# Kernel tuning notes

Hardware: AMD Instinct MI355X
Metric: run time of the kernel (lower is better)

The kernel has to match this reference:

```python
import jax, jax.numpy as jnp
import numpy as np

KEY_DIM = 1024
VALUE_DIM = 1024
NUM_HEADS = 16
ORIGIN_SHAPE = (8, 16, 16)  # T, H, W video-token grid
LOCAL_BLOCKS = 3
B = 1
S = int(np.prod(ORIGIN_SHAPE))  # 2048
DH = KEY_DIM // NUM_HEADS       # 64
DV = VALUE_DIM // NUM_HEADS


def make_layout():
    """Vectorized equivalent of SparseAttention.make_layout (causal=True)."""
    shape = np.array(ORIGIN_SHAPE, dtype=np.int64)
    cum = np.concatenate([np.flip(np.cumprod(np.flip(shape)))[1:], [1]]).astype(np.int64)
    idx = np.arange(S, dtype=np.int64)
    coords = (idx[None, :] // cum[:, None]) % shape[:, None]  # [ndim, S]
    diff = idx[:, None] - idx[None, :]
    layout = (diff >= 0) & (diff <= LOCAL_BLOCKS)  # causal local window
    for d in range(len(ORIGIN_SHAPE) - 1):  # causal axial strides along dims 0..ndim-2
        same = np.ones((S, S), dtype=bool)
        for e in range(len(ORIGIN_SHAPE)):
            if e != d:
                same &= coords[e][:, None] == coords[e][None, :]
        layout |= same & (coords[d][None, :] <= coords[d][:, None])
    return layout  # [S, S] bool


def setup_inputs() -> dict:
    key = jax.random.key(0)
    ks = jax.random.split(key, 11)
    sc = 0.02
    inp = {
        "query": jax.random.normal(ks[0], (B, S, KEY_DIM), jnp.float32),
        "key":   jax.random.normal(ks[1], (B, S, KEY_DIM), jnp.float32),
        "value": jax.random.normal(ks[2], (B, S, VALUE_DIM), jnp.float32),
        "wq": sc * jax.random.normal(ks[3], (KEY_DIM, KEY_DIM), jnp.float32),
        "bq": jnp.zeros((KEY_DIM,), jnp.float32),
        "wk": sc * jax.random.normal(ks[4], (KEY_DIM, KEY_DIM), jnp.float32),
        "bk": jnp.zeros((KEY_DIM,), jnp.float32),
        "wv": sc * jax.random.normal(ks[5], (VALUE_DIM, VALUE_DIM), jnp.float32),
        "bv": jnp.zeros((VALUE_DIM,), jnp.float32),
        "wo": sc * jax.random.normal(ks[6], (VALUE_DIM, KEY_DIM), jnp.float32),
        "bo": jnp.zeros((KEY_DIM,), jnp.float32),
        "layout": jnp.asarray(make_layout(), jnp.int32)[None, None],  # [1,1,S,S]
    }
    return inp


def reference(query, key, value, wq, bq, wk, bk, wv, bv, wo, bo, layout):
    def split(x, d):  # [B,S,H*d] -> [B,H,S,d]
        return x.reshape(B, S, NUM_HEADS, d).transpose(0, 2, 1, 3)
    q = split(query @ wq + bq, DH)
    k = split(key @ wk + bk, DH)
    v = split(value @ wv + bv, DV)
    logits = jnp.einsum('bhsd,bhtd->bhst', q, k) / jnp.sqrt(jnp.float32(DH))
    logits = jnp.where(layout > 0, logits, jnp.float32(-1e9))
    attn = jax.nn.softmax(logits, axis=-1)  # matches tf.sparse.softmax over layout support
    out = jnp.einsum('bhst,bhtd->bhsd', attn, v)
    out = out.transpose(0, 2, 1, 3).reshape(B, S, VALUE_DIM)
    return out @ wo + bo
```

## Files before the change

kernel.cpp:

```cpp
#include <hip/hip_runtime.h>
#include <hip/hip_bf16.h>
#include <cstdint>
#include <math.h>

#define SEQ    2048
#define DMODEL 1024
#define NHEAD  16
#define DHEAD  64
#define NZPAD  32

typedef __bf16 bf16;
typedef __bf16 bf16x8 __attribute__((ext_vector_type(8)));
typedef float  f32x4  __attribute__((ext_vector_type(4)));

typedef __attribute__((address_space(3))) uint32_t lds_u32;
typedef __attribute__((address_space(1))) const uint32_t global_u32;

__device__ __forceinline__ void async_load16(const void* g, void* l) {
    __builtin_amdgcn_global_load_lds((global_u32*)g, (lds_u32*)l, 16, 0, 0);
}

#define CAST_BLOCKS 3072
#define TR_BLOCKS   4096
#define NZ_BLOCKS   256

__global__ __launch_bounds__(256) void prep_kernel(
    const float* __restrict__ q, const float* __restrict__ k, const float* __restrict__ v,
    bf16* __restrict__ qx, bf16* __restrict__ kx, bf16* __restrict__ vx,
    const float* __restrict__ w0, const float* __restrict__ w1,
    const float* __restrict__ w2, const float* __restrict__ w3,
    bf16* __restrict__ t0, bf16* __restrict__ t1,
    bf16* __restrict__ t2, bf16* __restrict__ t3,
    int* __restrict__ nzidx, int* __restrict__ nzcnt) {
    __shared__ float tile[32][33];
    const int bid = blockIdx.x;
    if (bid < CAST_BLOCKS) {
        const int z = bid >> 10;
        const float* src = (z == 0) ? q : (z == 1) ? k : v;
        bf16* dst        = (z == 0) ? qx : (z == 1) ? kx : vx;
        const int i = (bid & 1023) * 256 + threadIdx.x;
        const float4* s4 = (const float4*)src;
        float4 a = s4[i * 2 + 0];
        float4 b = s4[i * 2 + 1];
        bf16x8 o;
        o[0] = (bf16)a.x; o[1] = (bf16)a.y; o[2] = (bf16)a.z; o[3] = (bf16)a.w;
        o[4] = (bf16)b.x; o[5] = (bf16)b.y; o[6] = (bf16)b.z; o[7] = (bf16)b.w;
        ((bf16x8*)dst)[i] = o;
    } else if (bid < CAST_BLOCKS + TR_BLOCKS) {
        const int b = bid - CAST_BLOCKS;
        const int z = b >> 10, rem = b & 1023;
        const float* w = (z == 0) ? w0 : (z == 1) ? w1 : (z == 2) ? w2 : w3;
        bf16* t        = (z == 0) ? t0 : (z == 1) ? t1 : (z == 2) ? t2 : t3;
        const int tx = threadIdx.x & 31, ty = threadIdx.x >> 5;
        const int kbase = (rem >> 5) * 32, nbase = (rem & 31) * 32;
#pragma unroll
        for (int i = 0; i < 4; ++i)
            tile[ty + 8 * i][tx] = w[(size_t)(kbase + ty + 8 * i) * DMODEL + nbase + tx];
        __syncthreads();
#pragma unroll
        for (int i = 0; i < 4; ++i)
            t[(size_t)(nbase + ty + 8 * i) * DMODEL + kbase + tx] = (bf16)tile[tx][ty + 8 * i];
    } else {
        const int b = bid - CAST_BLOCKS - TR_BLOCKS;
        const int g = threadIdx.x >> 5, l = threadIdx.x & 31;
        const int s = b * 8 + g;
        const int t = (s >> 8) & 7, h = (s >> 4) & 15, w = s & 15;
        const int win = (s < 3) ? s : 3;
        const int cnt = t + h + win + 1;
        int j;
        if (l < t)            j = l * 256 + h * 16 + w;
        else if (l < t + h)   j = t * 256 + (l - t) * 16 + w;
        else if (l < cnt)     j = s - (cnt - 1 - l);
        else                  j = s;
        nzidx[s * NZPAD + l] = j;
        if (l == 0) nzcnt[s] = cnt;
    }
}

template <int TM, typename OutT>
__device__ __forceinline__ void gemm_bt_body(
    const bf16* __restrict__ A, const bf16* __restrict__ BT,
    const float* __restrict__ bias, OutT* __restrict__ C) {
    constexpr int K = 1024, N = 1024;
    constexpr int BK = 64;
    constexpr int MI = TM / 32;
    constexpr int ACH = TM * (BK / 8);
    constexpr int BCH = 128 * (BK / 8);
    constexpr int TCH = ACH + BCH;
    __shared__ bf16 sA[2][TM * BK];
    __shared__ bf16 sB[2][128 * BK];
    const int tid = threadIdx.x;
    const int w = tid >> 6, lane = tid & 63;
    const int wm = w >> 1, wn = w & 1;
    const int lr = lane & 15, quad = lane >> 4;
    const int m0 = blockIdx.y * TM, n0 = blockIdx.x * 128;

    f32x4 acc[MI][4] = {};
    float bia[4];
#pragma unroll
    for (int ni = 0; ni < 4; ++ni) bia[ni] = bias[n0 + wn * 64 + ni * 16 + lr];

    auto stage = [&](int buf, int kt) {
#pragma unroll
        for (int kk = 0; kk < TCH / 256; ++kk) {
            const int cb = kk * 256 + w * 64;
            const int p  = cb + lane;
            if (cb < ACH) {
                const int row = p >> 3, chl = p & 7;
                const int chg = chl ^ (row & 7);
                async_load16(A + (size_t)(m0 + row) * K + kt + chg * 8,
                             (char*)&sA[buf][0] + cb * 16);
            } else {
                const int p2 = p - ACH, row = p2 >> 3, chl = p2 & 7;
                const int chg = chl ^ (row & 7);
                async_load16(BT + (size_t)(n0 + row) * K + kt + chg * 8,
                             (char*)&sB[buf][0] + (cb - ACH) * 16);
            }
        }
    };

    stage(0, 0);
    stage(1, BK);
    int cur = 0;
    for (int kt = 0; kt < K; kt += BK) {
        if (kt + BK < K) {
            asm volatile("s_waitcnt vmcnt(6)" ::: "memory");
        } else {
            asm volatile("s_waitcnt vmcnt(0)" ::: "memory");
        }
        __builtin_amdgcn_s_barrier();
        __builtin_amdgcn_sched_barrier(0);
#pragma unroll
        for (int ks = 0; ks < 2; ++ks) {
            bf16x8 af[MI], bfr[4];
#pragma unroll
            for (int mi = 0; mi < MI; ++mi) {
                const int row = wm * (TM / 2) + mi * 16 + lr;
                af[mi] = *(const bf16x8*)
                    &sA[cur][row * BK + ((ks * 4 + quad) ^ (row & 7)) * 8];
            }
#pragma unroll
            for (int ni = 0; ni < 4; ++ni) {
                const int row = wn * 64 + ni * 16 + lr;
                bfr[ni] = *(const bf16x8*)
                    &sB[cur][row * BK + ((ks * 4 + quad) ^ (row & 7)) * 8];
            }
            __builtin_amdgcn_s_setprio(1);
#pragma unroll
            for (int mi = 0; mi < MI; ++mi)
#pragma unroll
                for (int ni = 0; ni < 4; ++ni)
                    acc[mi][ni] = __builtin_amdgcn_mfma_f32_16x16x32_bf16(
                        af[mi], bfr[ni], acc[mi][ni], 0, 0, 0);
            __builtin_amdgcn_s_setprio(0);
        }
        __builtin_amdgcn_s_barrier();
        __builtin_amdgcn_sched_barrier(0);
        if (kt + 2 * BK < K) stage(cur, kt + 2 * BK);
        cur ^= 1;
    }

#pragma unroll
    for (int mi = 0; mi < MI; ++mi)
#pragma unroll
        for (int ni = 0; ni < 4; ++ni) {
            const int row = m0 + wm * (TM / 2) + mi * 16 + quad * 4;
            const int col = n0 + wn * 64 + ni * 16 + lr;
            const f32x4 vv = acc[mi][ni];
#pragma unroll
            for (int r = 0; r < 4; ++r)
                C[(size_t)(row + r) * N + col] = (OutT)(vv[r] + bia[ni]);
        }
}

__global__ __launch_bounds__(256) void proj3_kernel(
    const bf16* qx, const bf16* kx, const bf16* vx,
    const bf16* wqT, const bf16* wkT, const bf16* wvT,
    const float* bq, const float* bk, const float* bv,
    bf16* qp, bf16* kp, bf16* vp) {
    const int z = blockIdx.z;
    const bf16* A  = (z == 0) ? qx : (z == 1) ? kx : vx;
    const bf16* BT = (z == 0) ? wqT : (z == 1) ? wkT : wvT;
    const float* b = (z == 0) ? bq : (z == 1) ? bk : bv;
    bf16* C        = (z == 0) ? qp : (z == 1) ? kp : vp;
    gemm_bt_body<64, bf16>(A, BT, b, C);
}

__global__ __launch_bounds__(256) void gemm_final_kernel(
    const bf16* A, const bf16* BT, const float* bias, float* C) {
    gemm_bt_body<64, float>(A, BT, bias, C);
}

__global__ __launch_bounds__(256) void attn_kernel(
    const bf16* __restrict__ qp, const bf16* __restrict__ kp, const bf16* __restrict__ vp,
    const int* __restrict__ nzidx, const int* __restrict__ nzcnt,
    bf16* __restrict__ ao) {
    const int wv = threadIdx.x >> 6, lane = threadIdx.x & 63;
    constexpr int NB = NHEAD * SEQ / 4;
    const int bid = (blockIdx.x & 7) * (NB >> 3) + (blockIdx.x >> 3);
    const int p = bid * 4 + wv;
    const int s = __builtin_amdgcn_readfirstlane(p & (SEQ - 1));
    const int h = __builtin_amdgcn_readfirstlane(p >> 11);
    const int hbase = h * DHEAD;
    const int hoff = hbase + lane;

    const int cnt = nzcnt[s];
    const int* idx = nzidx + s * NZPAD;
    int t[NZPAD];
#pragma unroll
    for (int c = 0; c < NZPAD; ++c) t[c] = idx[c];

    const int c_lane = lane & 31;
    const int fo = (lane >> 5) << 5;
    const int myT = idx[c_lane];

    const bf16x8* qrow = (const bf16x8*)(qp + (size_t)s * DMODEL + hbase + fo);
    const bf16x8* krow = (const bf16x8*)(kp + (size_t)myT * DMODEL + hbase + fo);
    bf16x8 qc[4], kc[4];
#pragma unroll
    for (int j = 0; j < 4; ++j) { qc[j] = qrow[j]; kc[j] = krow[j]; }

    float vvv[NZPAD];
#pragma unroll
    for (int c = 0; c < NZPAD; ++c)
        vvv[c] = (float)vp[(size_t)t[c] * DMODEL + hoff];

    float dot = 0.f;
#pragma unroll
    for (int j = 0; j < 4; ++j)
#pragma unroll
        for (int e = 0; e < 8; ++e)
            dot = fmaf((float)qc[j][e], (float)kc[j][e], dot);
    dot += __shfl_xor(dot, 32);

    const float logit = (c_lane < cnt) ? dot * 0.125f : -1e30f;
    float m = logit;
    m = fmaxf(m, __shfl_xor(m, 1)); m = fmaxf(m, __shfl_xor(m, 2));
    m = fmaxf(m, __shfl_xor(m, 4)); m = fmaxf(m, __shfl_xor(m, 8));
    m = fmaxf(m, __shfl_xor(m, 16));
    const float e = __expf(logit - m);
    float ssum = e;
    ssum += __shfl_xor(ssum, 1); ssum += __shfl_xor(ssum, 2);
    ssum += __shfl_xor(ssum, 4); ssum += __shfl_xor(ssum, 8);
    ssum += __shfl_xor(ssum, 16);
    const float prob = e / ssum;

    float acc = 0.f;
#pragma unroll
    for (int c = 0; c < NZPAD; ++c) {
        const float pc = __uint_as_float(
            __builtin_amdgcn_readlane(__float_as_uint(prob), c));
        acc = fmaf(pc, vvv[c], acc);
    }
    ao[(size_t)s * DMODEL + hoff] = (bf16)acc;
}

extern "C" void kernel_launch(void* const* d_in, const int* in_sizes, int n_in,
                              void* d_out, int out_size, void* d_ws, size_t ws_size,
                              hipStream_t stream) {
    const float* query = (const float*)d_in[0];
    const float* key   = (const float*)d_in[1];
    const float* value = (const float*)d_in[2];
    const float* wq = (const float*)d_in[3];
    const float* bq = (const float*)d_in[4];
    const float* wk = (const float*)d_in[5];
    const float* bk = (const float*)d_in[6];
    const float* wv = (const float*)d_in[7];
    const float* bv = (const float*)d_in[8];
    const float* wo = (const float*)d_in[9];
    const float* bo = (const float*)d_in[10];
    float* out = (float*)d_out;

    char* ws = (char*)d_ws;
    auto alloc = [&](size_t bytes) {
        char* p = ws;
        ws += (bytes + 255) & ~(size_t)255;
        return p;
    };
    bf16* qx  = (bf16*)alloc((size_t)SEQ * DMODEL * 2);
    bf16* kx  = (bf16*)alloc((size_t)SEQ * DMODEL * 2);
    bf16* vx  = (bf16*)alloc((size_t)SEQ * DMODEL * 2);
    bf16* wqT = (bf16*)alloc((size_t)DMODEL * DMODEL * 2);
    bf16* wkT = (bf16*)alloc((size_t)DMODEL * DMODEL * 2);
    bf16* wvT = (bf16*)alloc((size_t)DMODEL * DMODEL * 2);
    bf16* woT = (bf16*)alloc((size_t)DMODEL * DMODEL * 2);
    bf16* qp  = (bf16*)alloc((size_t)SEQ * DMODEL * 2);
    bf16* kp  = (bf16*)alloc((size_t)SEQ * DMODEL * 2);
    bf16* vp  = (bf16*)alloc((size_t)SEQ * DMODEL * 2);
    bf16* ao  = (bf16*)alloc((size_t)SEQ * DMODEL * 2);
    int* nzidx = (int*)alloc((size_t)SEQ * NZPAD * 4);
    int* nzcnt = (int*)alloc((size_t)SEQ * 4);

    prep_kernel<<<dim3(CAST_BLOCKS + TR_BLOCKS + NZ_BLOCKS), 256, 0, stream>>>(
        query, key, value, qx, kx, vx,
        wq, wk, wv, wo, wqT, wkT, wvT, woT,
        nzidx, nzcnt);
    proj3_kernel<<<dim3(8, 32, 3), 256, 0, stream>>>(
        qx, kx, vx, wqT, wkT, wvT, bq, bk, bv, qp, kp, vp);
    attn_kernel<<<dim3(NHEAD * SEQ / 4), 256, 0, stream>>>(qp, kp, vp, nzidx, nzcnt, ao);
    gemm_final_kernel<<<dim3(8, 32), 256, 0, stream>>>(ao, woT, bo, out);
}
```

Before: 169.8 us.

## Fuse fp32-to-bf16 activation cast into projection GEMM and compute sparse indices inline

Removes the separate activation cast pass: the projection GEMM now loads fp32 query/key/value through registers, converts them to bf16 and writes them into swizzled LDS, while weights still stream in via async LDS loads. The sparse-support index table is no longer precomputed; the attention kernel derives each index arithmetically from the token coordinates. The weight transpose uses 64x64 tiles with vectorized float4 reads and bf16x4 writes, and the output GEMM uses 32-row tiles to double its block count. The trade-off is a shallower prefetch (one stage ahead with full waits each iteration) and register-staged A loads, which may expose more memory latency in the GEMMs.

```diff
diff --git a/kernel.cpp b/kernel.cpp
--- a/kernel.cpp
+++ b/kernel.cpp
@@ -10,6 +10,7 @@
 #define NZPAD  32
 
 typedef __bf16 bf16;
+typedef __bf16 bf16x4 __attribute__((ext_vector_type(4)));
 typedef __bf16 bf16x8 __attribute__((ext_vector_type(8)));
 typedef float  f32x4  __attribute__((ext_vector_type(4)));
 
@@ -20,73 +21,55 @@
     __builtin_amdgcn_global_load_lds((global_u32*)g, (lds_u32*)l, 16, 0, 0);
 }
 
-#define CAST_BLOCKS 3072
-#define TR_BLOCKS   4096
-#define NZ_BLOCKS   256
-
-__global__ __launch_bounds__(256) void prep_kernel(
-    const float* __restrict__ q, const float* __restrict__ k, const float* __restrict__ v,
-    bf16* __restrict__ qx, bf16* __restrict__ kx, bf16* __restrict__ vx,
+__device__ __forceinline__ int support_idx(int s, int c, int tt, int hh,
+                                           int cnt) {
+    const int jA = c * 256 + (s & 255);
+    const int jB = (s & 0x700) + (c - tt) * 16 + (s & 15);
+    const int jC = s - (cnt - 1 - c);
+    return c < tt ? jA : (c < tt + hh ? jB : (c < cnt ? jC : s));
+}
+
+__global__ __launch_bounds__(256) void prep_tr_kernel(
     const float* __restrict__ w0, const float* __restrict__ w1,
     const float* __restrict__ w2, const float* __restrict__ w3,
     bf16* __restrict__ t0, bf16* __restrict__ t1,
-    bf16* __restrict__ t2, bf16* __restrict__ t3,
-    int* __restrict__ nzidx, int* __restrict__ nzcnt) {
-    __shared__ float tile[32][33];
-    const int bid = blockIdx.x;
-    if (bid < CAST_BLOCKS) {
-        const int z = bid >> 10;
-        const float* src = (z == 0) ? q : (z == 1) ? k : v;
-        bf16* dst        = (z == 0) ? qx : (z == 1) ? kx : vx;
-        const int i = (bid & 1023) * 256 + threadIdx.x;
-        const float4* s4 = (const float4*)src;
-        float4 a = s4[i * 2 + 0];
-        float4 b = s4[i * 2 + 1];
-        bf16x8 o;
-        o[0] = (bf16)a.x; o[1] = (bf16)a.y; o[2] = (bf16)a.z; o[3] = (bf16)a.w;
-        o[4] = (bf16)b.x; o[5] = (bf16)b.y; o[6] = (bf16)b.z; o[7] = (bf16)b.w;
-        ((bf16x8*)dst)[i] = o;
-    } else if (bid < CAST_BLOCKS + TR_BLOCKS) {
-        const int b = bid - CAST_BLOCKS;
-        const int z = b >> 10, rem = b & 1023;
-        const float* w = (z == 0) ? w0 : (z == 1) ? w1 : (z == 2) ? w2 : w3;
-        bf16* t        = (z == 0) ? t0 : (z == 1) ? t1 : (z == 2) ? t2 : t3;
-        const int tx = threadIdx.x & 31, ty = threadIdx.x >> 5;
-        const int kbase = (rem >> 5) * 32, nbase = (rem & 31) * 32;
-#pragma unroll
-        for (int i = 0; i < 4; ++i)
-            tile[ty + 8 * i][tx] = w[(size_t)(kbase + ty + 8 * i) * DMODEL + nbase + tx];
-        __syncthreads();
-#pragma unroll
-        for (int i = 0; i < 4; ++i)
-            t[(size_t)(nbase + ty + 8 * i) * DMODEL + kbase + tx] = (bf16)tile[tx][ty + 8 * i];
-    } else {
-        const int b = bid - CAST_BLOCKS - TR_BLOCKS;
-        const int g = threadIdx.x >> 5, l = threadIdx.x & 31;
-        const int s = b * 8 + g;
-        const int t = (s >> 8) & 7, h = (s >> 4) & 15, w = s & 15;
-        const int win = (s < 3) ? s : 3;
-        const int cnt = t + h + win + 1;
-        int j;
-        if (l < t)            j = l * 256 + h * 16 + w;
-        else if (l < t + h)   j = t * 256 + (l - t) * 16 + w;
-        else if (l < cnt)     j = s - (cnt - 1 - l);
-        else                  j = s;
-        nzidx[s * NZPAD + l] = j;
-        if (l == 0) nzcnt[s] = cnt;
-    }
-}
-
-template <int TM, typename OutT>
-__device__ __forceinline__ void gemm_bt_body(
-    const bf16* __restrict__ A, const bf16* __restrict__ BT,
-    const float* __restrict__ bias, OutT* __restrict__ C) {
-    constexpr int K = 1024, N = 1024;
-    constexpr int BK = 64;
-    constexpr int MI = TM / 32;
-    constexpr int ACH = TM * (BK / 8);
-    constexpr int BCH = 128 * (BK / 8);
-    constexpr int TCH = ACH + BCH;
+    bf16* __restrict__ t2, bf16* __restrict__ t3) {
+    __shared__ float tile[64][65];
+    const int z = blockIdx.x >> 8, rem = blockIdx.x & 255;
+    const float* w = (z == 0) ? w0 : (z == 1) ? w1 : (z == 2) ? w2 : w3;
+    bf16* t        = (z == 0) ? t0 : (z == 1) ? t1 : (z == 2) ? t2 : t3;
+    const int kb = (rem >> 4) * 64, nb = (rem & 15) * 64;
+    const int c4 = threadIdx.x & 15, rg = threadIdx.x >> 4;
+#pragma unroll
+    for (int i = 0; i < 4; ++i) {
+        const int row = rg * 4 + i;
+        const float4 v = *(const float4*)&w[(size_t)(kb + row) * DMODEL + nb + c4 * 4];
+        tile[row][c4 * 4 + 0] = v.x; tile[row][c4 * 4 + 1] = v.y;
+        tile[row][c4 * 4 + 2] = v.z; tile[row][c4 * 4 + 3] = v.w;
+    }
+    __syncthreads();
+#pragma unroll
+    for (int i = 0; i < 4; ++i) {
+        const int n = rg * 4 + i;
+        bf16x4 o;
+        o[0] = (bf16)tile[c4 * 4 + 0][n]; o[1] = (bf16)tile[c4 * 4 + 1][n];
+        o[2] = (bf16)tile[c4 * 4 + 2][n]; o[3] = (bf16)tile[c4 * 4 + 3][n];
+        *(bf16x4*)&t[(size_t)(nb + n) * DMODEL + kb + c4 * 4] = o;
+    }
+}
+
+__global__ __launch_bounds__(256) void proj3_kernel(
+    const float* __restrict__ qf, const float* __restrict__ kf, const float* __restrict__ vf,
+    const bf16* __restrict__ wqT, const bf16* __restrict__ wkT, const bf16* __restrict__ wvT,
+    const float* __restrict__ bq, const float* __restrict__ bk, const float* __restrict__ bv,
+    bf16* __restrict__ qp, bf16* __restrict__ kp, bf16* __restrict__ vp) {
+    constexpr int K = 1024, N = 1024, BK = 64, TM = 64, MI = 2;
+    const int z = blockIdx.z;
+    const float* A  = (z == 0) ? qf : (z == 1) ? kf : vf;
+    const bf16* BT  = (z == 0) ? wqT : (z == 1) ? wkT : wvT;
+    const float* bi = (z == 0) ? bq : (z == 1) ? bk : bv;
+    bf16* C         = (z == 0) ? qp : (z == 1) ? kp : vp;
+
     __shared__ bf16 sA[2][TM * BK];
     __shared__ bf16 sB[2][128 * BK];
     const int tid = threadIdx.x;
@@ -94,17 +77,120 @@
     const int wm = w >> 1, wn = w & 1;
     const int lr = lane & 15, quad = lane >> 4;
     const int m0 = blockIdx.y * TM, n0 = blockIdx.x * 128;
+    const int ar = tid >> 2, ak4 = tid & 3;
 
     f32x4 acc[MI][4] = {};
     float bia[4];
 #pragma unroll
+    for (int ni = 0; ni < 4; ++ni) bia[ni] = bi[n0 + wn * 64 + ni * 16 + lr];
+
+    float4 av[4];
+    auto issueA = [&](int kt) {
+        const float4* src = (const float4*)(A + (size_t)(m0 + ar) * K + kt + ak4 * 16);
+#pragma unroll
+        for (int i = 0; i < 4; ++i) av[i] = src[i];
+    };
+    auto writeA = [&](int buf) {
+        bf16x8 c0, c1;
+        c0[0] = (bf16)av[0].x; c0[1] = (bf16)av[0].y; c0[2] = (bf16)av[0].z; c0[3] = (bf16)av[0].w;
+        c0[4] = (bf16)av[1].x; c0[5] = (bf16)av[1].y; c0[6] = (bf16)av[1].z; c0[7] = (bf16)av[1].w;
+        c1[0] = (bf16)av[2].x; c1[1] = (bf16)av[2].y; c1[2] = (bf16)av[2].z; c1[3] = (bf16)av[2].w;
+        c1[4] = (bf16)av[3].x; c1[5] = (bf16)av[3].y; c1[6] = (bf16)av[3].z; c1[7] = (bf16)av[3].w;
+        const int s0 = (ak4 * 2) ^ (ar & 7), s1 = (ak4 * 2 + 1) ^ (ar & 7);
+        *(bf16x8*)&sA[buf][ar * BK + s0 * 8] = c0;
+        *(bf16x8*)&sA[buf][ar * BK + s1 * 8] = c1;
+    };
+    auto gloadB = [&](int buf, int kt) {
+#pragma unroll
+        for (int kk = 0; kk < 4; ++kk) {
+            const int cb = kk * 256 + w * 64;
+            const int p = cb + lane;
+            const int row = p >> 3, chl = p & 7;
+            const int chg = chl ^ (row & 7);
+            async_load16(BT + (size_t)(n0 + row) * K + kt + chg * 8,
+                         (char*)&sB[buf][0] + cb * 16);
+        }
+    };
+
+    issueA(0);
+    gloadB(0, 0);
+    writeA(0);
+    asm volatile("s_waitcnt vmcnt(0) lgkmcnt(0)" ::: "memory");
+    __builtin_amdgcn_s_barrier();
+    __builtin_amdgcn_sched_barrier(0);
+
+    int cur = 0;
+    for (int kt = 0; kt < K; kt += BK) {
+        const bool more = (kt + BK) < K;
+        if (more) { issueA(kt + BK); gloadB(cur ^ 1, kt + BK); }
+#pragma unroll
+        for (int ks = 0; ks < 2; ++ks) {
+            bf16x8 af[MI], bfr[4];
+#pragma unroll
+            for (int mi = 0; mi < MI; ++mi) {
+                const int row = wm * (TM / 2) + mi * 16 + lr;
+                af[mi] = *(const bf16x8*)
+                    &sA[cur][row * BK + ((ks * 4 + quad) ^ (row & 7)) * 8];
+            }
+#pragma unroll
+            for (int ni = 0; ni < 4; ++ni) {
+                const int row = wn * 64 + ni * 16 + lr;
+                bfr[ni] = *(const bf16x8*)
+                    &sB[cur][row * BK + ((ks * 4 + quad) ^ (row & 7)) * 8];
+            }
+            __builtin_amdgcn_s_setprio(1);
+#pragma unroll
+            for (int mi = 0; mi < MI; ++mi)
+#pragma unroll
+                for (int ni = 0; ni < 4; ++ni)
+                    acc[mi][ni] = __builtin_amdgcn_mfma_f32_16x16x32_bf16(
+                        af[mi], bfr[ni], acc[mi][ni], 0, 0, 0);
+            __builtin_amdgcn_s_setprio(0);
+        }
+        if (more) writeA(cur ^ 1);
+        asm volatile("s_waitcnt vmcnt(0) lgkmcnt(0)" ::: "memory");
+        __builtin_amdgcn_s_barrier();
+        __builtin_amdgcn_sched_barrier(0);
+        cur ^= 1;
+    }
+
+#pragma unroll
+    for (int mi = 0; mi < MI; ++mi)
+#pragma unroll
+        for (int ni = 0; ni < 4; ++ni) {
+            const int row = m0 + wm * (TM / 2) + mi * 16 + quad * 4;
+            const int col = n0 + wn * 64 + ni * 16 + lr;
+            const f32x4 vv = acc[mi][ni];
+#pragma unroll
+            for (int r = 0; r < 4; ++r)
+                C[(size_t)(row + r) * N + col] = (bf16)(vv[r] + bia[ni]);
+        }
+}
+
+__global__ __launch_bounds__(256) void gemm_final_kernel(
+    const bf16* __restrict__ A, const bf16* __restrict__ BT,
+    const float* __restrict__ bias, float* __restrict__ C) {
+    constexpr int K = 1024, N = 1024, BK = 64, TM = 32, MI = 1;
+    constexpr int ACH = TM * (BK / 8);
+    constexpr int TCH = ACH + 128 * (BK / 8);
+    __shared__ bf16 sA[2][TM * BK];
+    __shared__ bf16 sB[2][128 * BK];
+    const int tid = threadIdx.x;
+    const int w = tid >> 6, lane = tid & 63;
+    const int wm = w >> 1, wn = w & 1;
+    const int lr = lane & 15, quad = lane >> 4;
+    const int m0 = blockIdx.y * TM, n0 = blockIdx.x * 128;
+
+    f32x4 acc[MI][4] = {};
+    float bia[4];
+#pragma unroll
     for (int ni = 0; ni < 4; ++ni) bia[ni] = bias[n0 + wn * 64 + ni * 16 + lr];
 
     auto stage = [&](int buf, int kt) {
 #pragma unroll
         for (int kk = 0; kk < TCH / 256; ++kk) {
             const int cb = kk * 256 + w * 64;
-            const int p  = cb + lane;
+            const int p = cb + lane;
             if (cb < ACH) {
                 const int row = p >> 3, chl = p & 7;
                 const int chg = chl ^ (row & 7);
@@ -120,16 +206,13 @@
     };
 
     stage(0, 0);
-    stage(1, BK);
+    asm volatile("s_waitcnt vmcnt(0)" ::: "memory");
+    __builtin_amdgcn_s_barrier();
+    __builtin_amdgcn_sched_barrier(0);
+
     int cur = 0;
     for (int kt = 0; kt < K; kt += BK) {
-        if (kt + BK < K) {
-            asm volatile("s_waitcnt vmcnt(6)" ::: "memory");
-        } else {
-            asm volatile("s_waitcnt vmcnt(0)" ::: "memory");
-        }
-        __builtin_amdgcn_s_barrier();
-        __builtin_amdgcn_sched_barrier(0);
+        if (kt + BK < K) stage(cur ^ 1, kt + BK);
 #pragma unroll
         for (int ks = 0; ks < 2; ++ks) {
             bf16x8 af[MI], bfr[4];
@@ -154,9 +237,9 @@
                         af[mi], bfr[ni], acc[mi][ni], 0, 0, 0);
             __builtin_amdgcn_s_setprio(0);
         }
+        asm volatile("s_waitcnt vmcnt(0)" ::: "memory");
         __builtin_amdgcn_s_barrier();
         __builtin_amdgcn_sched_barrier(0);
-        if (kt + 2 * BK < K) stage(cur, kt + 2 * BK);
         cur ^= 1;
     }
 
@@ -169,31 +252,12 @@
             const f32x4 vv = acc[mi][ni];
 #pragma unroll
             for (int r = 0; r < 4; ++r)
-                C[(size_t)(row + r) * N + col] = (OutT)(vv[r] + bia[ni]);
-        }
-}
-
-__global__ __launch_bounds__(256) void proj3_kernel(
-    const bf16* qx, const bf16* kx, const bf16* vx,
-    const bf16* wqT, const bf16* wkT, const bf16* wvT,
-    const float* bq, const float* bk, const float* bv,
-    bf16* qp, bf16* kp, bf16* vp) {
-    const int z = blockIdx.z;
-    const bf16* A  = (z == 0) ? qx : (z == 1) ? kx : vx;
-    const bf16* BT = (z == 0) ? wqT : (z == 1) ? wkT : wvT;
-    const float* b = (z == 0) ? bq : (z == 1) ? bk : bv;
-    bf16* C        = (z == 0) ? qp : (z == 1) ? kp : vp;
-    gemm_bt_body<64, bf16>(A, BT, b, C);
-}
-
-__global__ __launch_bounds__(256) void gemm_final_kernel(
-    const bf16* A, const bf16* BT, const float* bias, float* C) {
-    gemm_bt_body<64, float>(A, BT, bias, C);
+                C[(size_t)(row + r) * N + col] = vv[r] + bia[ni];
+        }
 }
 
 __global__ __launch_bounds__(256) void attn_kernel(
     const bf16* __restrict__ qp, const bf16* __restrict__ kp, const bf16* __restrict__ vp,
-    const int* __restrict__ nzidx, const int* __restrict__ nzcnt,
     bf16* __restrict__ ao) {
     const int wv = threadIdx.x >> 6, lane = threadIdx.x & 63;
     constexpr int NB = NHEAD * SEQ / 4;
@@ -204,15 +268,17 @@
     const int hbase = h * DHEAD;
     const int hoff = hbase + lane;
 
-    const int cnt = nzcnt[s];
-    const int* idx = nzidx + s * NZPAD;
+    const int tt = (s >> 8) & 7, hh = (s >> 4) & 15;
+    const int win = (s < 3) ? s : 3;
+    const int cnt = tt + hh + win + 1;
+
     int t[NZPAD];
 #pragma unroll
-    for (int c = 0; c < NZPAD; ++c) t[c] = idx[c];
+    for (int c = 0; c < NZPAD; ++c) t[c] = support_idx(s, c, tt, hh, cnt);
 
     const int c_lane = lane & 31;
     const int fo = (lane >> 5) << 5;
-    const int myT = idx[c_lane];
+    const int myT = support_idx(s, c_lane, tt, hh, cnt);
 
     const bf16x8* qrow = (const bf16x8*)(qp + (size_t)s * DMODEL + hbase + fo);
     const bf16x8* krow = (const bf16x8*)(kp + (size_t)myT * DMODEL + hbase + fo);
@@ -277,9 +343,6 @@
         ws += (bytes + 255) & ~(size_t)255;
         return p;
     };
-    bf16* qx  = (bf16*)alloc((size_t)SEQ * DMODEL * 2);
-    bf16* kx  = (bf16*)alloc((size_t)SEQ * DMODEL * 2);
-    bf16* vx  = (bf16*)alloc((size_t)SEQ * DMODEL * 2);
     bf16* wqT = (bf16*)alloc((size_t)DMODEL * DMODEL * 2);
     bf16* wkT = (bf16*)alloc((size_t)DMODEL * DMODEL * 2);
     bf16* wvT = (bf16*)alloc((size_t)DMODEL * DMODEL * 2);
@@ -288,15 +351,11 @@
     bf16* kp  = (bf16*)alloc((size_t)SEQ * DMODEL * 2);
     bf16* vp  = (bf16*)alloc((size_t)SEQ * DMODEL * 2);
     bf16* ao  = (bf16*)alloc((size_t)SEQ * DMODEL * 2);
-    int* nzidx = (int*)alloc((size_t)SEQ * NZPAD * 4);
-    int* nzcnt = (int*)alloc((size_t)SEQ * 4);
-
-    prep_kernel<<<dim3(CAST_BLOCKS + TR_BLOCKS + NZ_BLOCKS), 256, 0, stream>>>(
-        query, key, value, qx, kx, vx,
-        wq, wk, wv, wo, wqT, wkT, wvT, woT,
-        nzidx, nzcnt);
+
+    prep_tr_kernel<<<dim3(1024), 256, 0, stream>>>(
+        wq, wk, wv, wo, wqT, wkT, wvT, woT);
     proj3_kernel<<<dim3(8, 32, 3), 256, 0, stream>>>(
-        qx, kx, vx, wqT, wkT, wvT, bq, bk, bv, qp, kp, vp);
-    attn_kernel<<<dim3(NHEAD * SEQ / 4), 256, 0, stream>>>(qp, kp, vp, nzidx, nzcnt, ao);
-    gemm_final_kernel<<<dim3(8, 32), 256, 0, stream>>>(ao, woT, bo, out);
-}
+        query, key, value, wqT, wkT, wvT, bq, bk, bv, qp, kp, vp);
+    attn_kernel<<<dim3(NHEAD * SEQ / 4), 256, 0, stream>>>(qp, kp, vp, ao);
+    gemm_final_kernel<<<dim3(8, 64), 256, 0, stream>>>(ao, woT, bo, out);
+}
```

Result: no change. 172.3 us (+1.5%).
